# Kernel optimization log

Measured on AMD Instinct MI355X. Metric: run time of the kernel, lower is better.

Reference implementation:

```python
import jax, jax.numpy as jnp
import numpy as np

B, N, C, H = 2, 2048, 1024, 16
D = C // H  # head_dim = 64


def setup_inputs() -> dict:
    key = jax.random.key(0)
    ks = jax.random.split(key, 5)
    s = 1.0 / np.sqrt(C)
    return {
        "q": jax.random.normal(ks[0], (B, N, C), dtype=jnp.float32),
        "W_qkv": jax.random.normal(ks[1], (C, 3 * C), dtype=jnp.float32) * s,
        "b_qkv": jnp.zeros((3 * C,), dtype=jnp.float32),
        "W_proj": jax.random.normal(ks[2], (C, C), dtype=jnp.float32) * s,
        "b_proj": jnp.zeros((C,), dtype=jnp.float32),
    }


def reference(q, W_qkv, b_qkv, W_proj, b_proj):
    # Self-attention: k = v = q. Full 3C projection (as in the torch code).
    qkv = q @ W_qkv + b_qkv  # [B, N, 3C]
    qh = qkv[:, :, :C].reshape(B, N, H, D)
    kh = qkv[:, :, C:2 * C].reshape(B, N, H, D)
    vh = qkv[:, :, 2 * C:].reshape(B, N, H, D)
    scale = D ** -0.5
    # [B, H, N, N] attention logits
    attn = jnp.einsum("bnhd,bmhd->bhnm", qh, kh) * scale
    attn = jax.nn.softmax(attn, axis=-1)
    out = jnp.einsum("bhnm,bmhd->bnhd", attn, vh).reshape(B, N, C)
    return out @ W_proj + b_proj
```

## Files before the change

kernel.cpp:

```cpp
#include <hip/hip_runtime.h>
#include <stdint.h>

typedef __bf16 bf16_t;
typedef __bf16 bf16x8 __attribute__((ext_vector_type(8)));
typedef __bf16 bf16x4 __attribute__((ext_vector_type(4)));
typedef float f32x4 __attribute__((ext_vector_type(4)));

#define L2E 1.44269504088896340736f
#define QSCALE (0.125f * L2E)

__device__ __forceinline__ void gload16(const bf16_t* g, bf16_t* l) {
  __builtin_amdgcn_global_load_lds(
      (const __attribute__((address_space(1))) void*)g,
      (__attribute__((address_space(3))) void*)l, 16, 0, 0);
}

__device__ __forceinline__ float fexp2(float x) {
  float r;
  asm("v_exp_f32 %0, %1" : "=v"(r) : "v"(x));
  return r;
}

__global__ __launch_bounds__(256) void prep_kernel(const float* __restrict__ qin,
                                                   bf16_t* __restrict__ qbf,
                                                   const float* __restrict__ wqkv,
                                                   bf16_t* __restrict__ wqkv_t,
                                                   const float* __restrict__ wproj,
                                                   bf16_t* __restrict__ wproj_t) {
  __shared__ float tile[64][65];
  const int bid = blockIdx.x, t = threadIdx.x;
  if (bid < 4096) {
    int i = bid * 256 + t;
    float4 v = reinterpret_cast<const float4*>(qin)[i];
    bf16x4 o;
    o[0] = (bf16_t)v.x; o[1] = (bf16_t)v.y; o[2] = (bf16_t)v.z; o[3] = (bf16_t)v.w;
    reinterpret_cast<bf16x4*>(qbf)[i] = o;
    return;
  }
  const float* in; bf16_t* out; int N, bx, by;
  if (bid < 4864) {
    int bb = bid - 4096; in = wqkv; out = wqkv_t; N = 3072; bx = bb % 48; by = bb / 48;
  } else {
    int bb = bid - 4864; in = wproj; out = wproj_t; N = 1024; bx = bb % 16; by = bb / 16;
  }
  const int K = 1024;
  int k0 = by * 64, n0 = bx * 64;
  int r = t >> 4, c4 = (t & 15) * 4;
#pragma unroll
  for (int rr = 0; rr < 4; rr++) {
    int row = r + rr * 16;
    float4 v = *reinterpret_cast<const float4*>(&in[(size_t)(k0 + row) * N + n0 + c4]);
    tile[row][c4 + 0] = v.x; tile[row][c4 + 1] = v.y;
    tile[row][c4 + 2] = v.z; tile[row][c4 + 3] = v.w;
  }
  __syncthreads();
#pragma unroll
  for (int rr = 0; rr < 4; rr++) {
    int nr = r + rr * 16;
    bf16x4 o;
#pragma unroll
    for (int i = 0; i < 4; i++) o[i] = (bf16_t)tile[c4 + i][nr];
    *reinterpret_cast<bf16x4*>(&out[(size_t)(n0 + nr) * K + k0 + c4]) = o;
  }
}

template <int MODE, int BM>
__global__ __launch_bounds__(256) void gemm_kernel(const bf16_t* __restrict__ A,
                                                   const bf16_t* __restrict__ Bt,
                                                   const float* __restrict__ bias,
                                                   void* __restrict__ out,
                                                   bf16_t* __restrict__ vT,
                                                   int K, int gm, int gn, int ldo) {
  constexpr int ACH = BM / 8;
  constexpr int NCH = ACH + 16;
  constexpr int CPW = NCH / 4;
  constexpr int IR = BM / 32;
  constexpr int SMEM = (MODE == 0) ? 17408 : (BM * 64 + 8192);
  __shared__ __align__(16) bf16_t smem[SMEM];
  bf16_t* At = smem;
  bf16_t* Bts = smem + BM * 64;
  const int t = threadIdx.x, lane = t & 63, w = t >> 6;
  const int g = lane >> 4, q = lane & 15;
  const int bid = blockIdx.x, x = bid & 7, r = bid >> 3;
  const int qm = gm >> 2, qn = gn >> 1;
  const int lm = r % qm, ln = r / qm;
  const int m0 = ((x & 3) * qm + lm) * BM, n0 = ((x >> 2) * qn + ln) * 128;
  const int wm = (w >> 1) * (BM / 2), wn = (w & 1) * 64;

  const bf16_t* srcp[CPW]; int dsto[CPW];
#pragma unroll
  for (int i = 0; i < CPW; i++) {
    int cI = i * 4 + w;
    bool isA = cI < ACH;
    int row = (isA ? cI : cI - ACH) * 8 + (lane >> 3);
    int p = (lane & 7) ^ (row & 7);
    srcp[i] = (isA ? A + (size_t)(m0 + row) * K : Bt + (size_t)(n0 + row) * K) + p * 8;
    dsto[i] = (isA ? cI * 512 : BM * 64 + (cI - ACH) * 512);
  }

  f32x4 acc[IR][4];
#pragma unroll
  for (int i = 0; i < IR; i++)
#pragma unroll
    for (int j = 0; j < 4; j++) acc[i][j] = (f32x4){0.f, 0.f, 0.f, 0.f};

  for (int k0 = 0; k0 < K; k0 += 64) {
    __syncthreads();
#pragma unroll
    for (int i = 0; i < CPW; i++) gload16(srcp[i] + k0, &smem[dsto[i]]);
    __syncthreads();
#pragma unroll
    for (int dc = 0; dc < 2; dc++) {
      bf16x8 am[IR], bn[4];
#pragma unroll
      for (int i = 0; i < IR; i++) {
        int ra = wm + 16 * i + q;
        am[i] = *reinterpret_cast<const bf16x8*>(&At[ra * 64 + ((dc * 32 + g * 8) ^ ((ra & 7) * 8))]);
      }
#pragma unroll
      for (int j = 0; j < 4; j++) {
        int rb = wn + 16 * j + q;
        bn[j] = *reinterpret_cast<const bf16x8*>(&Bts[rb * 64 + ((dc * 32 + g * 8) ^ ((rb & 7) * 8))]);
      }
#pragma unroll
      for (int i = 0; i < IR; i++)
#pragma unroll
        for (int j = 0; j < 4; j++)
          acc[i][j] = __builtin_amdgcn_mfma_f32_16x16x32_bf16(am[i], bn[j], acc[i][j], 0, 0, 0);
    }
  }

  if (MODE == 0 && n0 >= 2048) {
    __syncthreads();
    bf16_t* TT = smem;
#pragma unroll
    for (int i = 0; i < IR; i++)
#pragma unroll
      for (int j = 0; j < 4; j++)
#pragma unroll
        for (int rr = 0; rr < 4; rr++) {
          int ch = wn + 16 * j + q;
          int tok = wm + 16 * i + 4 * g + rr;
          float v = acc[i][j][rr] + bias[n0 + ch];
          TT[ch * 136 + (((tok >> 3) ^ (ch & 7)) * 8) + (tok & 7)] = (bf16_t)v;
        }
    __syncthreads();
    const int bb = m0 >> 11;
    const int t0 = m0 & 2047;
#pragma unroll
    for (int it = 0; it < 8; it++) {
      int ch = it * 16 + w * 4 + (lane >> 4);
      int ck = lane & 15;
      uint4 val = *reinterpret_cast<const uint4*>(&TT[ch * 136 + ((ck ^ (ch & 7)) * 8)]);
      int vch = (n0 - 2048) + ch;
      bf16_t* dst = vT + ((size_t)(bb * 16 + (vch >> 6)) * 64 + (vch & 63)) * 2048 + t0 + ck * 8;
      *reinterpret_cast<uint4*>(dst) = val;
    }
  } else if (MODE == 0) {
    const float sc = (n0 < 1024) ? QSCALE : 1.0f;
    __syncthreads();
    bf16_t* TT = smem;
#pragma unroll
    for (int i = 0; i < IR; i++)
#pragma unroll
      for (int j = 0; j < 4; j++)
#pragma unroll
        for (int rr = 0; rr < 4; rr++) {
          int ch = wn + 16 * j + q;
          int tok = wm + 16 * i + 4 * g + rr;
          float v = (acc[i][j][rr] + bias[n0 + ch]) * sc;
          TT[tok * 136 + (((ch >> 3) ^ (tok & 7)) * 8) + (ch & 7)] = (bf16_t)v;
        }
    __syncthreads();
#pragma unroll
    for (int it = 0; it < 8; it++) {
      int tok = it * 16 + (t >> 4);
      int gr = t & 15;
      uint4 val = *reinterpret_cast<const uint4*>(&TT[tok * 136 + ((gr ^ (tok & 7)) * 8)]);
      bf16_t* dst = (bf16_t*)out + (size_t)(m0 + tok) * ldo + n0 + gr * 8;
      *reinterpret_cast<uint4*>(dst) = val;
    }
  } else {
#pragma unroll
    for (int i = 0; i < IR; i++)
#pragma unroll
      for (int j = 0; j < 4; j++)
#pragma unroll
        for (int rr = 0; rr < 4; rr++) {
          int row = m0 + wm + 16 * i + 4 * g + rr;
          int col = n0 + wn + 16 * j + q;
          ((float*)out)[(size_t)row * ldo + col] = acc[i][j][rr] + bias[col];
        }
  }
}

__global__ __launch_bounds__(256) void attn_kernel(const bf16_t* __restrict__ qk,
                                                   const bf16_t* __restrict__ vT,
                                                   bf16_t* __restrict__ aout) {
  __shared__ __align__(16) bf16_t sK[2][4096];
  __shared__ __align__(16) bf16_t sV[2][4096];
  __shared__ __align__(16) bf16_t sP[4][1024];

  const int t = threadIdx.x, lane = t & 63, w = t >> 6;
  const int g = lane >> 4, q = lane & 15;
  const int bid = blockIdx.x, xr = bid >> 3;
  const int bh = (bid & 7) * 4 + (xr >> 5);
  const int b = bh >> 4, h = bh & 15;
  const int q0 = (xr & 31) * 64 + w * 16;
  const bf16_t* qk_b = qk + (size_t)b * 2048 * 2048;
  const bf16_t* vT_h = vT + (size_t)bh * 64 * 2048;
  bf16_t* Pw = sP[w];

  const bf16_t* srcK[2]; const bf16_t* srcV[2]; int dsto[2];
#pragma unroll
  for (int i = 0; i < 2; i++) {
    int gI = (w * 2 + i) * 64 + lane;
    int row = gI >> 3, p = (gI & 7) ^ (row & 7);
    srcK[i] = qk_b + (size_t)row * 2048 + 1024 + h * 64 + p * 8;
    srcV[i] = vT_h + (size_t)row * 2048 + p * 8;
    dsto[i] = (w * 2 + i) * 512;
  }

  bf16x8 bq[2];
  {
    const bf16_t* qr = qk_b + (size_t)(q0 + q) * 2048 + h * 64;
    bq[0] = *reinterpret_cast<const bf16x8*>(qr + g * 8);
    bq[1] = *reinterpret_cast<const bf16x8*>(qr + 32 + g * 8);
  }

  bf16x8 ones;
#pragma unroll
  for (int i = 0; i < 8; i++) ones[i] = (bf16_t)1.0f;

  f32x4 oacc[4];
#pragma unroll
  for (int c = 0; c < 4; c++) oacc[c] = (f32x4){0.f, 0.f, 0.f, 0.f};
  f32x4 lacc = (f32x4){0.f, 0.f, 0.f, 0.f};

#pragma unroll
  for (int i = 0; i < 2; i++) {
    gload16(srcK[i], &sK[0][dsto[i]]);
    gload16(srcV[i], &sV[0][dsto[i]]);
  }
  __syncthreads();

  for (int tt = 0; tt < 32; tt++) {
    const int cur = tt & 1;
    if (tt + 1 < 32) {
      size_t koffK = (size_t)(tt + 1) * 64 * 2048;
      size_t koffV = (size_t)(tt + 1) * 64;
#pragma unroll
      for (int i = 0; i < 2; i++) {
        gload16(srcK[i] + koffK, &sK[cur ^ 1][dsto[i]]);
        gload16(srcV[i] + koffV, &sV[cur ^ 1][dsto[i]]);
      }
    }

    const bf16_t* Kc = sK[cur];
    f32x4 s[4];
#pragma unroll
    for (int c = 0; c < 4; c++) {
      int row = 16 * c + q, sw = (q & 7) * 8;
      bf16x8 ka0 = *reinterpret_cast<const bf16x8*>(&Kc[row * 64 + ((g * 8) ^ sw)]);
      bf16x8 ka1 = *reinterpret_cast<const bf16x8*>(&Kc[row * 64 + ((32 + g * 8) ^ sw)]);
      f32x4 z = (f32x4){0.f, 0.f, 0.f, 0.f};
      z = __builtin_amdgcn_mfma_f32_16x16x32_bf16(ka0, bq[0], z, 0, 0, 0);
      z = __builtin_amdgcn_mfma_f32_16x16x32_bf16(ka1, bq[1], z, 0, 0, 0);
      s[c] = z;
    }

#pragma unroll
    for (int c = 0; c < 4; c++) {
      bf16x4 pk;
#pragma unroll
      for (int rr = 0; rr < 4; rr++) pk[rr] = (bf16_t)fexp2(s[c][rr]);
      *reinterpret_cast<bf16x4*>(
          &Pw[q * 64 + (((2 * c + (g >> 1)) ^ (q & 7)) * 8) + (g & 1) * 4]) = pk;
    }

    const bf16_t* Vc = sV[cur];
#pragma unroll
    for (int kc = 0; kc < 2; kc++) {
      bf16x8 pb = *reinterpret_cast<const bf16x8*>(
          &Pw[q * 64 + (((kc * 4 + g) ^ (q & 7)) * 8)]);
      lacc = __builtin_amdgcn_mfma_f32_16x16x32_bf16(ones, pb, lacc, 0, 0, 0);
#pragma unroll
      for (int c = 0; c < 4; c++) {
        int row = 16 * c + q;
        bf16x8 va = *reinterpret_cast<const bf16x8*>(
            &Vc[row * 64 + (((kc * 4 + g) ^ (q & 7)) * 8)]);
        oacc[c] = __builtin_amdgcn_mfma_f32_16x16x32_bf16(va, pb, oacc[c], 0, 0, 0);
      }
    }

    __syncthreads();
  }

  float inv = 1.0f / lacc[0];
  bf16_t* orow = aout + (size_t)(b * 2048 + q0 + q) * 1024 + h * 64;
#pragma unroll
  for (int c = 0; c < 4; c++) {
    bf16x4 ov;
#pragma unroll
    for (int rr = 0; rr < 4; rr++) ov[rr] = (bf16_t)(oacc[c][rr] * inv);
    *reinterpret_cast<bf16x4*>(orow + c * 16 + g * 4) = ov;
  }
}

extern "C" void kernel_launch(void* const* d_in, const int* in_sizes, int n_in,
                              void* d_out, int out_size, void* d_ws, size_t ws_size,
                              hipStream_t stream) {
  const float* q     = (const float*)d_in[0];
  const float* Wqkv  = (const float*)d_in[1];
  const float* bqkv  = (const float*)d_in[2];
  const float* Wproj = (const float*)d_in[3];
  const float* bproj = (const float*)d_in[4];
  float* out = (float*)d_out;

  char* ws = (char*)d_ws;
  bf16_t* q_bf    = (bf16_t*)(ws);
  bf16_t* wqkv_t  = (bf16_t*)(ws + 8388608);
  bf16_t* wproj_t = (bf16_t*)(ws + 14680064);
  bf16_t* qk      = (bf16_t*)(ws + 16777216);
  bf16_t* vT      = (bf16_t*)(ws + 33554432);
  bf16_t* aout    = q_bf;

  prep_kernel<<<5120, 256, 0, stream>>>(q, q_bf, Wqkv, wqkv_t, Wproj, wproj_t);
  gemm_kernel<0, 128><<<768, 256, 0, stream>>>(q_bf, wqkv_t, bqkv, qk, vT, 1024, 32, 24, 2048);
  attn_kernel<<<1024, 256, 0, stream>>>(qk, vT, aout);
  gemm_kernel<1, 64><<<512, 256, 0, stream>>>(aout, wproj_t, bproj, out, nullptr, 1024, 64, 8, 1024);
}
```

Measured before the change: 131.0 us.

## Replace output projection GEMM with 128x128 tiles and intra-block split-K

The output projection moves from a 64x128-tile kernel with 512 blocks of 256 threads to a dedicated kernel using 128x128 tiles, 256 blocks of 512 threads. Each block splits K in two halves across two warp groups and reduces the partial sums through shared memory before adding bias and writing fp32 output. The intent is more reuse per loaded tile and fewer total loads, while keeping enough waves in flight. The cost is a larger LDS footprint (about 66 KB), an extra reduction pass, and fewer blocks to spread across CUs. The generic GEMM template drops its MODE 1 path.

```diff
diff --git a/kernel.cpp b/kernel.cpp
--- a/kernel.cpp
+++ b/kernel.cpp
@@ -75,7 +75,7 @@
   constexpr int NCH = ACH + 16;
   constexpr int CPW = NCH / 4;
   constexpr int IR = BM / 32;
-  constexpr int SMEM = (MODE == 0) ? 17408 : (BM * 64 + 8192);
+  constexpr int SMEM = 17408;
   __shared__ __align__(16) bf16_t smem[SMEM];
   bf16_t* At = smem;
   bf16_t* Bts = smem + BM * 64;
@@ -130,7 +130,7 @@
     }
   }
 
-  if (MODE == 0 && n0 >= 2048) {
+  if (n0 >= 2048) {
     __syncthreads();
     bf16_t* TT = smem;
 #pragma unroll
@@ -156,7 +156,7 @@
       bf16_t* dst = vT + ((size_t)(bb * 16 + (vch >> 6)) * 64 + (vch & 63)) * 2048 + t0 + ck * 8;
       *reinterpret_cast<uint4*>(dst) = val;
     }
-  } else if (MODE == 0) {
+  } else {
     const float sc = (n0 < 1024) ? QSCALE : 1.0f;
     __syncthreads();
     bf16_t* TT = smem;
@@ -180,16 +180,92 @@
       bf16_t* dst = (bf16_t*)out + (size_t)(m0 + tok) * ldo + n0 + gr * 8;
       *reinterpret_cast<uint4*>(dst) = val;
     }
-  } else {
-#pragma unroll
-    for (int i = 0; i < IR; i++)
+  }
+}
+
+__global__ __launch_bounds__(512) void gemm_proj(const bf16_t* __restrict__ A,
+                                                 const bf16_t* __restrict__ Bt,
+                                                 const float* __restrict__ bias,
+                                                 float* __restrict__ out) {
+  __shared__ __align__(16) bf16_t smem[33280];
+  const int K = 1024;
+  const int t = threadIdx.x, lane = t & 63, w = t >> 6;
+  const int g = lane >> 4, q = lane & 15;
+  const int kg = w >> 2, lw = w & 3;
+  const int bid = blockIdx.x, x = bid & 7, r = bid >> 3;
+  const int lm = r % 8, ln = r / 8;
+  const int m0 = ((x & 3) * 8 + lm) * 128, n0 = ((x >> 2) * 4 + ln) * 128;
+  const int wm = (lw >> 1) * 64, wn = (lw & 1) * 64;
+  bf16_t* At = smem + kg * 16384;
+  bf16_t* Bts = smem + kg * 16384 + 8192;
+
+  const bf16_t* srcp[8]; int dsto[8];
+#pragma unroll
+  for (int i = 0; i < 8; i++) {
+    int cI = i * 4 + lw;
+    bool isA = cI < 16;
+    int row = (isA ? cI : cI - 16) * 8 + (lane >> 3);
+    int p = (lane & 7) ^ (row & 7);
+    srcp[i] = (isA ? A + (size_t)(m0 + row) * K : Bt + (size_t)(n0 + row) * K)
+              + kg * 512 + p * 8;
+    dsto[i] = kg * 16384 + (isA ? cI * 512 : 8192 + (cI - 16) * 512);
+  }
+
+  f32x4 acc[4][4];
+#pragma unroll
+  for (int i = 0; i < 4; i++)
+#pragma unroll
+    for (int j = 0; j < 4; j++) acc[i][j] = (f32x4){0.f, 0.f, 0.f, 0.f};
+
+  for (int k0 = 0; k0 < 512; k0 += 64) {
+    __syncthreads();
+#pragma unroll
+    for (int i = 0; i < 8; i++) gload16(srcp[i] + k0, &smem[dsto[i]]);
+    __syncthreads();
+#pragma unroll
+    for (int dc = 0; dc < 2; dc++) {
+      bf16x8 am[4], bn[4];
+#pragma unroll
+      for (int i = 0; i < 4; i++) {
+        int ra = wm + 16 * i + q;
+        am[i] = *reinterpret_cast<const bf16x8*>(&At[ra * 64 + ((dc * 32 + g * 8) ^ ((ra & 7) * 8))]);
+      }
+#pragma unroll
+      for (int j = 0; j < 4; j++) {
+        int rb = wn + 16 * j + q;
+        bn[j] = *reinterpret_cast<const bf16x8*>(&Bts[rb * 64 + ((dc * 32 + g * 8) ^ ((rb & 7) * 8))]);
+      }
+#pragma unroll
+      for (int i = 0; i < 4; i++)
+#pragma unroll
+        for (int j = 0; j < 4; j++)
+          acc[i][j] = __builtin_amdgcn_mfma_f32_16x16x32_bf16(am[i], bn[j], acc[i][j], 0, 0, 0);
+    }
+  }
+
+  __syncthreads();
+  float* red = (float*)smem;
+  if (kg == 1) {
+#pragma unroll
+    for (int i = 0; i < 4; i++)
 #pragma unroll
       for (int j = 0; j < 4; j++)
 #pragma unroll
+        for (int rr = 0; rr < 4; rr++)
+          red[(wm + 16 * i + 4 * g + rr) * 130 + wn + 16 * j + q] = acc[i][j][rr];
+  }
+  __syncthreads();
+  if (kg == 0) {
+#pragma unroll
+    for (int i = 0; i < 4; i++)
+#pragma unroll
+      for (int j = 0; j < 4; j++)
+#pragma unroll
         for (int rr = 0; rr < 4; rr++) {
-          int row = m0 + wm + 16 * i + 4 * g + rr;
-          int col = n0 + wn + 16 * j + q;
-          ((float*)out)[(size_t)row * ldo + col] = acc[i][j][rr] + bias[col];
+          int row = wm + 16 * i + 4 * g + rr;
+          int col = wn + 16 * j + q;
+          out[(size_t)(m0 + row) * 1024 + n0 + col] =
+              acc[i][j][rr] + red[row * 130 + col] + bias[n0 + col];
         }
   }
 }
@@ -328,5 +404,5 @@
   prep_kernel<<<5120, 256, 0, stream>>>(q, q_bf, Wqkv, wqkv_t, Wproj, wproj_t);
   gemm_kernel<0, 128><<<768, 256, 0, stream>>>(q_bf, wqkv_t, bqkv, qk, vT, 1024, 32, 24, 2048);
   attn_kernel<<<1024, 256, 0, stream>>>(qk, vT, aout);
-  gemm_kernel<1, 64><<<512, 256, 0, stream>>>(aout, wproj_t, bproj, out, nullptr, 1024, 64, 8, 1024);
-}
+  gemm_proj<<<256, 512, 0, stream>>>(aout, wproj_t, bproj, out);
+}
```

Result: no change. 129.8 us (median of 2 runs) (-0.9%).
